# Optimization experiments

Measured on AMD Instinct MI355X. Metric: run time of the kernel, lower is better.

## Reference

```python
import jax, jax.numpy as jnp
import numpy as np

NUM_HEADS = 12
HEAD_DIM = 64
HIDDEN = 768
BATCH = 2
SEQ = 2048
NEG_BIG = 1e12


def _rope_tables(seq_len, dim, dtype=jnp.float32):
    # theta_i = 10000^(-2i/dim); sin/cos repeat-interleaved -> [seq_len, dim]
    half = dim // 2
    theta = jnp.power(10000.0, -jnp.arange(half, dtype=dtype) * (2.0 / dim))
    ang = jnp.arange(seq_len, dtype=dtype)[:, None] * theta[None, :]  # [n, half]
    sin_pos = jnp.repeat(jnp.sin(ang), 2, axis=-1)  # [n, dim]
    cos_pos = jnp.repeat(jnp.cos(ang), 2, axis=-1)
    return sin_pos, cos_pos


def setup_inputs() -> dict:
    key = jax.random.key(0)
    k1, k2, k3, k4 = jax.random.split(key, 4)
    inputs = jax.random.normal(k1, (BATCH, SEQ, HIDDEN), dtype=jnp.float32)
    mask = jax.random.randint(k2, (BATCH, SEQ), 0, 2, dtype=jnp.int32)
    # nn.Linear(hidden, num_heads*head_dim*2): weight [out, in], bias [out]
    W = jax.random.normal(k3, (NUM_HEADS * HEAD_DIM * 2, HIDDEN), dtype=jnp.float32) * (HIDDEN ** -0.5)
    b = jax.random.normal(k4, (NUM_HEADS * HEAD_DIM * 2,), dtype=jnp.float32) * 0.02
    return {"inputs": inputs, "mask": mask, "W": W, "b": b}


def reference(inputs, mask, W, b):
    B, N, _ = inputs.shape
    H, D = NUM_HEADS, HEAD_DIM
    hs = jnp.einsum('bnh,oh->bno', inputs, W) + b          # [B, N, 2*H*D]
    hs = hs.reshape(B, N, H, 2 * D)                        # split+stack -> [B, N, H, 2D]
    qw, kw = hs[..., :D], hs[..., D:]                      # [B, N, H, D]
    # qw2 = cat([-q_odd, q_even], -1) as in the torch code
    qw2 = jnp.concatenate([-qw[..., 1::2], qw[..., ::2]], axis=-1)
    kw2 = jnp.concatenate([-kw[..., 1::2], kw[..., ::2]], axis=-1)
    # permute to [B, H, N, D]
    qw, qw2 = qw.transpose(0, 2, 1, 3), qw2.transpose(0, 2, 1, 3)
    kw, kw2 = kw.transpose(0, 2, 1, 3), kw2.transpose(0, 2, 1, 3)
    sin_pos, cos_pos = _rope_tables(N, D, hs.dtype)        # [N, D], broadcasts over B, H
    qw = qw * cos_pos + qw2 * sin_pos
    kw = kw * cos_pos + kw2 * sin_pos
    logits = jnp.einsum('bhnd,bhmd->bhnm', qw, kw)         # [B, H, N, N]
    # padding mask over key axis: mask [B,N] -> [B,1,1,N]
    pad = mask.astype(logits.dtype)[:, None, None, :]
    logits = logits * pad - (1.0 - pad) * NEG_BIG
    # strictly-lower-triangular mask (keep upper triangle + diagonal)
    tril = jnp.tril(jnp.ones((N, N), dtype=logits.dtype), k=-1)
    logits = logits - tril * NEG_BIG
    return logits / (D ** 0.5)
```

## Files before the change

kernel.cpp:

```cpp
#include <hip/hip_runtime.h>
#include <hip/hip_bf16.h>
#include <cmath>

#define NH   12
#define HD   64
#define HID  768
#define NB   2
#define SEQL 2048
#define ROWS 4096
#define OUTW 1536

static constexpr float NEGBIG = 1000000000000.0f;

typedef __attribute__((ext_vector_type(4)))  float f32x4;
typedef __attribute__((ext_vector_type(8)))  short short8;
typedef __attribute__((ext_vector_type(16))) float f32x16;

__device__ __forceinline__ unsigned short f2bf(float f) {
    unsigned int u = __builtin_bit_cast(unsigned int, f);
    u += 0x7FFFu + ((u >> 16) & 1u);
    return (unsigned short)(u >> 16);
}

__device__ __forceinline__ void fill_tile(int fid, int tid,
                                          const int* __restrict__ mask,
                                          float* __restrict__ out) {
    const int bh = fid / 120;
    int j = fid % 120;
    int ntv = 1;
    while (j >= ntv) { j -= ntv; ++ntv; }
    const int nt = ntv, mt = j;
    const int bI = bh / NH;
    float* outbase = out + (size_t)bh * SEQL * SEQL;
    const int cg = tid & 31;
    const int r0 = tid >> 5;
    const int m0 = mt * 128 + cg * 4;
    const int4 mi = *reinterpret_cast<const int4*>(mask + bI * SEQL + m0);
    f32x4 v;
    v.x = ((float)mi.x - 2.0f) * (NEGBIG * 0.125f);
    v.y = ((float)mi.y - 2.0f) * (NEGBIG * 0.125f);
    v.z = ((float)mi.z - 2.0f) * (NEGBIG * 0.125f);
    v.w = ((float)mi.w - 2.0f) * (NEGBIG * 0.125f);
    float* ob = outbase + (size_t)(nt * 128) * SEQL + m0;
#pragma unroll
    for (int jj = 0; jj < 16; ++jj) {
        int row = r0 + 8 * jj;
        __builtin_nontemporal_store(v, reinterpret_cast<f32x4*>(ob + (size_t)row * SEQL));
    }
}

#define XQ (ROWS * HID / 4)
#define WQ (OUTW * HID / 4)
#define RQ (SEQL * 32)
#define PREP_BLOCKS 4480
#define FILL_PREP   400
#define FILL_P1     1800
__global__ void k_prep(const float* __restrict__ X, const float* __restrict__ W,
                       unsigned short* __restrict__ Xbf, unsigned short* __restrict__ Wbf,
                       float2* __restrict__ rtab,
                       const int* __restrict__ mask, float* __restrict__ out) {
    if (blockIdx.x >= PREP_BLOCKS) {
        fill_tile(blockIdx.x - PREP_BLOCKS, threadIdx.x, mask, out);
        return;
    }
    int i = blockIdx.x * blockDim.x + threadIdx.x;
    if (i < XQ + WQ) {
        const float* src = (i < XQ) ? X : W;
        unsigned short* dst = (i < XQ) ? Xbf : Wbf;
        int k = (i < XQ) ? i : i - XQ;
        float4 v = reinterpret_cast<const float4*>(src)[k];
        ushort4 o;
        o.x = f2bf(v.x); o.y = f2bf(v.y); o.z = f2bf(v.z); o.w = f2bf(v.w);
        reinterpret_cast<ushort4*>(dst)[k] = o;
    } else if (i < XQ + WQ + RQ) {
        int idx = i - (XQ + WQ);
        int n = idx >> 5, d = idx & 31;
        float theta = exp2f(-(float)d * (13.287712379549449f / 32.0f));
        float ang = (float)n * theta;
        rtab[idx] = make_float2(sinf(ang), cosf(ang));
    }
}

__global__ __launch_bounds__(256, 4) void k_proj_fill(
    const unsigned short* __restrict__ Xbf,
    const unsigned short* __restrict__ Wbf,
    const float*  __restrict__ bias,
    const float2* __restrict__ rtab,
    unsigned short* __restrict__ Qbf,
    unsigned short* __restrict__ Kbf,
    const int* __restrict__ mask,
    float* __restrict__ out)
{
    const int bid = blockIdx.x;
    const int tid = threadIdx.x;

    if (bid >= 768) {
        fill_tile(FILL_PREP + (bid - 768), tid, mask, out);
        return;
    }

    const int newbid = (bid & 7) * 96 + (bid >> 3);
    const int slab = newbid / 12;
    const int head = newbid % 12;
    const int row0 = slab * 64;
    const int lane = tid & 63;
    const int w    = tid >> 6;
    const int wr = w & 1, wc = w >> 1;
    const int l31 = lane & 31, lhi = lane >> 5;
    const int x7  = l31 & 7;

    __shared__ __align__(16) unsigned short smem[12288];

    f32x16 acc[2];
    {
        float bj0 = bias[head * 128 + wc * 64 + l31];
        float bj1 = bias[head * 128 + wc * 64 + 32 + l31];
#pragma unroll
        for (int r = 0; r < 16; ++r) { acc[0][r] = bj0; acc[1][r] = bj1; }
    }

    const unsigned short* Abase = Xbf + (size_t)row0 * HID;
    const unsigned short* Bbase = Wbf + (size_t)(head * 128) * HID;

    short8 ga[2], gb[4];
#pragma unroll
    for (int r = 0; r < 2; ++r) {
        int idx = tid + 256 * r, row = idx >> 3, s = idx & 7;
        ga[r] = *reinterpret_cast<const short8*>(Abase + (size_t)row * HID + s * 8);
    }
#pragma unroll
    for (int r = 0; r < 4; ++r) {
        int idx = tid + 256 * r, row = idx >> 3, s = idx & 7;
        gb[r] = *reinterpret_cast<const short8*>(Bbase + (size_t)row * HID + s * 8);
    }
#pragma unroll
    for (int r = 0; r < 2; ++r) {
        int idx = tid + 256 * r, row = idx >> 3, s = idx & 7, ws = s ^ (row & 7);
        *reinterpret_cast<short8*>(smem + row * 64 + ws * 8) = ga[r];
    }
#pragma unroll
    for (int r = 0; r < 4; ++r) {
        int idx = tid + 256 * r, row = idx >> 3, s = idx & 7, ws = s ^ (row & 7);
        *reinterpret_cast<short8*>(smem + 4096 + row * 64 + ws * 8) = gb[r];
    }

    for (int t = 0; t < 12; ++t) {
        __syncthreads();
        if (t < 11) {
            const int kk = (t + 1) * 64;
#pragma unroll
            for (int r = 0; r < 2; ++r) {
                int idx = tid + 256 * r, row = idx >> 3, s = idx & 7;
                ga[r] = *reinterpret_cast<const short8*>(Abase + (size_t)row * HID + kk + s * 8);
            }
#pragma unroll
            for (int r = 0; r < 4; ++r) {
                int idx = tid + 256 * r, row = idx >> 3, s = idx & 7;
                gb[r] = *reinterpret_cast<const short8*>(Bbase + (size_t)row * HID + kk + s * 8);
            }
        }
#pragma unroll
        for (int ks = 0; ks < 4; ++ks) {
            int sl = (ks * 2 + lhi) ^ x7;
            short8 a  = *reinterpret_cast<const short8*>(smem + (wr * 32 + l31) * 64 + sl * 8);
            short8 b0 = *reinterpret_cast<const short8*>(smem + 4096 + (wc * 64 + l31) * 64 + sl * 8);
            short8 b1 = *reinterpret_cast<const short8*>(smem + 4096 + (wc * 64 + 32 + l31) * 64 + sl * 8);
            acc[0] = __builtin_amdgcn_mfma_f32_32x32x16_bf16(a, b0, acc[0], 0, 0, 0);
            acc[1] = __builtin_amdgcn_mfma_f32_32x32x16_bf16(a, b1, acc[1], 0, 0, 0);
        }
        if (t < 11) {
            __syncthreads();
#pragma unroll
            for (int r = 0; r < 2; ++r) {
                int idx = tid + 256 * r, row = idx >> 3, s = idx & 7, ws = s ^ (row & 7);
                *reinterpret_cast<short8*>(smem + row * 64 + ws * 8) = ga[r];
            }
#pragma unroll
            for (int r = 0; r < 4; ++r) {
                int idx = tid + 256 * r, row = idx >> 3, s = idx & 7, ws = s ^ (row & 7);
                *reinterpret_cast<short8*>(smem + 4096 + row * 64 + ws * 8) = gb[r];
            }
        }
    }
    __syncthreads();

    float (*hs)[132] = reinterpret_cast<float (*)[132]>(smem);
    for (int s = 0; s < 2; ++s) {
        if (wr == s) {
#pragma unroll
            for (int j = 0; j < 2; ++j)
#pragma unroll
                for (int r = 0; r < 16; ++r) {
                    int rr = (r & 3) + 8 * (r >> 2) + 4 * lhi;
                    hs[rr][wc * 64 + j * 32 + l31] = acc[j][r];
                }
        }
        __syncthreads();
#pragma unroll 4
        for (int it = 0; it < 8; ++it) {
            int f   = tid + 256 * it;
            int row = f >> 6;
            int u   = f & 63;
            int isK = u >> 5;
            int dp  = u & 31;
            int d0  = 2 * dp, d1 = d0 + 1;
            int cb  = isK * 64;
            int grow = row0 + s * 32 + row;
            int bI = grow >> 11;
            int n  = grow & 2047;
            float2 sc = rtab[n * 32 + dp];
            float v0 = hs[row][cb + d0];
            float v1 = hs[row][cb + d1];
            int p0 = (d0 < 32) ? (2 * d0 + 1) : (2 * d0 - 64);
            int p1 = (d1 < 32) ? (2 * d1 + 1) : (2 * d1 - 64);
            float pv0 = hs[row][cb + p0];
            float pv1 = hs[row][cb + p1];
            float sg0 = (d0 < 32) ? -1.0f : 1.0f;
            float sg1 = (d1 < 32) ? -1.0f : 1.0f;
            ushort2 st;
            st.x = f2bf(v0 * sc.y + sg0 * pv0 * sc.x);
            st.y = f2bf(v1 * sc.y + sg1 * pv1 * sc.x);
            unsigned short* dst = isK ? (unsigned short*)Kbf : (unsigned short*)Qbf;
            size_t idx = ((size_t)(bI * NH + head) * SEQL + n) * HD + d0;
            *reinterpret_cast<ushort2*>(dst + idx) = st;
        }
        __syncthreads();
    }
}

__global__ __launch_bounds__(256) void k_logits(
    const unsigned short* __restrict__ Qbf,
    const unsigned short* __restrict__ Kbf,
    const int* __restrict__ mask,
    float* __restrict__ out)
{
    const int bid = blockIdx.x;
    const int newbid = (bid & 7) * 493 + (bid >> 3);
    const int tid = threadIdx.x;

    if (newbid >= 3264) {
        fill_tile(FILL_PREP + FILL_P1 + (newbid - 3264), tid, mask, out);
        return;
    }

    const int bh = newbid / 136;
    int j = newbid % 136;
    int ntv = 0;
    while (j >= 16 - ntv) { j -= 16 - ntv; ++ntv; }
    const int nt = ntv, mt = ntv + j;
    const int bI = bh / NH;
    float* outbase = out + (size_t)bh * SEQL * SEQL;

    const int lane = tid & 63;
    const int w = tid >> 6;
    const int rowHalf = w & 1, colHalf = w >> 1;
    const int l31 = lane & 31, lhi = lane >> 5;
    const int n0 = nt * 128 + rowHalf * 64;
    const int m0 = mt * 128 + colHalf * 64;

    f32x16 acc[2][2];
#pragma unroll
    for (int i = 0; i < 2; ++i)
#pragma unroll
        for (int jj = 0; jj < 2; ++jj)
#pragma unroll
            for (int r = 0; r < 16; ++r) acc[i][jj][r] = 0.0f;

    const unsigned short* Aq = Qbf + ((size_t)bh * SEQL + n0 + l31) * HD + 8 * lhi;
    const unsigned short* Bk = Kbf + ((size_t)bh * SEQL + m0 + l31) * HD + 8 * lhi;
#pragma unroll
    for (int t2 = 0; t2 < 4; ++t2) {
        short8 a0 = *reinterpret_cast<const short8*>(Aq + 16 * t2);
        short8 a1 = *reinterpret_cast<const short8*>(Aq + 32 * HD + 16 * t2);
        short8 b0 = *reinterpret_cast<const short8*>(Bk + 16 * t2);
        short8 b1 = *reinterpret_cast<const short8*>(Bk + 32 * HD + 16 * t2);
        acc[0][0] = __builtin_amdgcn_mfma_f32_32x32x16_bf16(a0, b0, acc[0][0], 0, 0, 0);
        acc[0][1] = __builtin_amdgcn_mfma_f32_32x32x16_bf16(a0, b1, acc[0][1], 0, 0, 0);
        acc[1][0] = __builtin_amdgcn_mfma_f32_32x32x16_bf16(a1, b0, acc[1][0], 0, 0, 0);
        acc[1][1] = __builtin_amdgcn_mfma_f32_32x32x16_bf16(a1, b1, acc[1][1], 0, 0, 0);
    }

    __shared__ float tl[64][128];
#pragma unroll
    for (int i = 0; i < 2; ++i) {
#pragma unroll
        for (int jj = 0; jj < 2; ++jj) {
#pragma unroll
            for (int r = 0; r < 16; ++r) {
                int rr = (r & 3) + 8 * (r >> 2) + 4 * lhi;
                tl[rowHalf * 32 + rr][colHalf * 64 + jj * 32 + l31] = acc[i][jj][r];
            }
        }
        __syncthreads();
#pragma unroll
        for (int it = 0; it < 8; ++it) {
            int f   = tid + 256 * it;
            int lr  = f >> 5;
            int cg  = f & 31;
            int grow = nt * 128 + (lr >> 5) * 64 + i * 32 + (lr & 31);
            int gcol = mt * 128 + cg * 4;
            const int4 mi = *reinterpret_cast<const int4*>(mask + bI * SEQL + gcol);
            f32x4 v = *reinterpret_cast<const f32x4*>(&tl[lr][cg * 4]);
            float pads[4] = {(float)mi.x, (float)mi.y, (float)mi.z, (float)mi.w};
#pragma unroll
            for (int e = 0; e < 4; ++e) {
                float vv = v[e] * pads[e] - (1.0f - pads[e]) * NEGBIG;
                if (gcol + e < grow) vv -= NEGBIG;
                v[e] = vv * 0.125f;
            }
            __builtin_nontemporal_store(v, reinterpret_cast<f32x4*>(outbase + (size_t)grow * SEQL + gcol));
        }
        __syncthreads();
    }
}

extern "C" void kernel_launch(void* const* d_in, const int* in_sizes, int n_in,
                              void* d_out, int out_size, void* d_ws, size_t ws_size,
                              hipStream_t stream) {
    const float* x    = (const float*)d_in[0];
    const int*   mask = (const int*)d_in[1];
    const float* W    = (const float*)d_in[2];
    const float* bias = (const float*)d_in[3];
    float* out = (float*)d_out;

    char* ws = (char*)d_ws;
    unsigned short* Xbf = (unsigned short*)(ws);
    unsigned short* Wbf = (unsigned short*)(ws + 6291456);
    unsigned short* Qbf = (unsigned short*)(ws + 8650752);
    unsigned short* Kbf = (unsigned short*)(ws + 14942208);
    float2*         rtab = (float2*)(ws + 21233664);

    k_prep<<<dim3(PREP_BLOCKS + FILL_PREP), dim3(256), 0, stream>>>(x, W, Xbf, Wbf, rtab, mask, out);
    k_proj_fill<<<dim3(768 + FILL_P1), dim3(256), 0, stream>>>(Xbf, Wbf, bias, rtab, Qbf, Kbf, mask, out);
    k_logits<<<dim3(3944), dim3(256), 0, stream>>>(Qbf, Kbf, mask, out);
}
```

Before: 90.52 us.

## Fuse X bf16 conversion into projection GEMM and rebalance fill tiles

The projection kernel now reads X directly as fp32 and converts it to bf16 on the fly while loading tiles, so the separate conversion pass and its 6 MB bf16 buffer are gone. The prep kernel only converts W and builds the rope table, which frees blocks for more masked-tile fills there and in the projection kernel. The logits kernel no longer carries any fill work. The trade-off is twice the global read bytes for X in the GEMM (each X tile is re-read per head) plus conversion ALU work in the load path.

```diff
diff --git a/kernel.cpp b/kernel.cpp
--- a/kernel.cpp
+++ b/kernel.cpp
@@ -20,6 +20,17 @@
     unsigned int u = __builtin_bit_cast(unsigned int, f);
     u += 0x7FFFu + ((u >> 16) & 1u);
     return (unsigned short)(u >> 16);
+}
+
+__device__ __forceinline__ short8 cvt8(const float* __restrict__ p) {
+    float4 v0 = *reinterpret_cast<const float4*>(p);
+    float4 v1 = *reinterpret_cast<const float4*>(p + 4);
+    short8 g;
+    g[0] = (short)f2bf(v0.x); g[1] = (short)f2bf(v0.y);
+    g[2] = (short)f2bf(v0.z); g[3] = (short)f2bf(v0.w);
+    g[4] = (short)f2bf(v1.x); g[5] = (short)f2bf(v1.y);
+    g[6] = (short)f2bf(v1.z); g[7] = (short)f2bf(v1.w);
+    return g;
 }
 
 __device__ __forceinline__ void fill_tile(int fid, int tid,
@@ -49,31 +60,26 @@
     }
 }
 
-#define XQ (ROWS * HID / 4)
 #define WQ (OUTW * HID / 4)
 #define RQ (SEQL * 32)
-#define PREP_BLOCKS 4480
-#define FILL_PREP   400
-#define FILL_P1     1800
-__global__ void k_prep(const float* __restrict__ X, const float* __restrict__ W,
-                       unsigned short* __restrict__ Xbf, unsigned short* __restrict__ Wbf,
-                       float2* __restrict__ rtab,
+#define PREP_BLOCKS 1408
+#define FILL_PREP   700
+#define FILL_P1     2180
+__global__ void k_prep(const float* __restrict__ W,
+                       unsigned short* __restrict__ Wbf, float2* __restrict__ rtab,
                        const int* __restrict__ mask, float* __restrict__ out) {
     if (blockIdx.x >= PREP_BLOCKS) {
         fill_tile(blockIdx.x - PREP_BLOCKS, threadIdx.x, mask, out);
         return;
     }
     int i = blockIdx.x * blockDim.x + threadIdx.x;
-    if (i < XQ + WQ) {
-        const float* src = (i < XQ) ? X : W;
-        unsigned short* dst = (i < XQ) ? Xbf : Wbf;
-        int k = (i < XQ) ? i : i - XQ;
-        float4 v = reinterpret_cast<const float4*>(src)[k];
+    if (i < WQ) {
+        float4 v = reinterpret_cast<const float4*>(W)[i];
         ushort4 o;
         o.x = f2bf(v.x); o.y = f2bf(v.y); o.z = f2bf(v.z); o.w = f2bf(v.w);
-        reinterpret_cast<ushort4*>(dst)[k] = o;
-    } else if (i < XQ + WQ + RQ) {
-        int idx = i - (XQ + WQ);
+        reinterpret_cast<ushort4*>(Wbf)[i] = o;
+    } else if (i < WQ + RQ) {
+        int idx = i - WQ;
         int n = idx >> 5, d = idx & 31;
         float theta = exp2f(-(float)d * (13.287712379549449f / 32.0f));
         float ang = (float)n * theta;
@@ -82,7 +88,7 @@
 }
 
 __global__ __launch_bounds__(256, 4) void k_proj_fill(
-    const unsigned short* __restrict__ Xbf,
+    const float* __restrict__ X,
     const unsigned short* __restrict__ Wbf,
     const float*  __restrict__ bias,
     const float2* __restrict__ rtab,
@@ -119,14 +125,14 @@
         for (int r = 0; r < 16; ++r) { acc[0][r] = bj0; acc[1][r] = bj1; }
     }
 
-    const unsigned short* Abase = Xbf + (size_t)row0 * HID;
+    const float* Abase = X + (size_t)row0 * HID;
     const unsigned short* Bbase = Wbf + (size_t)(head * 128) * HID;
 
     short8 ga[2], gb[4];
 #pragma unroll
     for (int r = 0; r < 2; ++r) {
         int idx = tid + 256 * r, row = idx >> 3, s = idx & 7;
-        ga[r] = *reinterpret_cast<const short8*>(Abase + (size_t)row * HID + s * 8);
+        ga[r] = cvt8(Abase + (size_t)row * HID + s * 8);
     }
 #pragma unroll
     for (int r = 0; r < 4; ++r) {
@@ -151,7 +157,7 @@
 #pragma unroll
             for (int r = 0; r < 2; ++r) {
                 int idx = tid + 256 * r, row = idx >> 3, s = idx & 7;
-                ga[r] = *reinterpret_cast<const short8*>(Abase + (size_t)row * HID + kk + s * 8);
+                ga[r] = cvt8(Abase + (size_t)row * HID + kk + s * 8);
             }
 #pragma unroll
             for (int r = 0; r < 4; ++r) {
@@ -235,13 +241,8 @@
     float* __restrict__ out)
 {
     const int bid = blockIdx.x;
-    const int newbid = (bid & 7) * 493 + (bid >> 3);
+    const int newbid = (bid & 7) * 408 + (bid >> 3);
     const int tid = threadIdx.x;
-
-    if (newbid >= 3264) {
-        fill_tile(FILL_PREP + FILL_P1 + (newbid - 3264), tid, mask, out);
-        return;
-    }
 
     const int bh = newbid / 136;
     int j = newbid % 136;
@@ -324,13 +325,12 @@
     float* out = (float*)d_out;
 
     char* ws = (char*)d_ws;
-    unsigned short* Xbf = (unsigned short*)(ws);
-    unsigned short* Wbf = (unsigned short*)(ws + 6291456);
-    unsigned short* Qbf = (unsigned short*)(ws + 8650752);
-    unsigned short* Kbf = (unsigned short*)(ws + 14942208);
-    float2*         rtab = (float2*)(ws + 21233664);
-
-    k_prep<<<dim3(PREP_BLOCKS + FILL_PREP), dim3(256), 0, stream>>>(x, W, Xbf, Wbf, rtab, mask, out);
-    k_proj_fill<<<dim3(768 + FILL_P1), dim3(256), 0, stream>>>(Xbf, Wbf, bias, rtab, Qbf, Kbf, mask, out);
-    k_logits<<<dim3(3944), dim3(256), 0, stream>>>(Qbf, Kbf, mask, out);
-}
+    unsigned short* Wbf = (unsigned short*)(ws);
+    unsigned short* Qbf = (unsigned short*)(ws + 2359296);
+    unsigned short* Kbf = (unsigned short*)(ws + 8650752);
+    float2*         rtab = (float2*)(ws + 14942208);
+
+    k_prep<<<dim3(PREP_BLOCKS + FILL_PREP), dim3(256), 0, stream>>>(W, Wbf, rtab, mask, out);
+    k_proj_fill<<<dim3(768 + FILL_P1), dim3(256), 0, stream>>>(x, Wbf, bias, rtab, Qbf, Kbf, mask, out);
+    k_logits<<<dim3(3264), dim3(256), 0, stream>>>(Qbf, Kbf, mask, out);
+}
```

Result: no change. 89.97 us (-0.6%).
